# Kernel optimization log

Measured on AMD Instinct MI355X. Metric: run time of the kernel, lower is better.

Reference implementation:

```python
import jax, jax.numpy as jnp
import numpy as np


def setup_inputs() -> dict:
    key = jax.random.key(0)
    k1, k2 = jax.random.split(key)
    ns, nd, n_classes = 16384, 2048, 1000
    x = jax.random.normal(k1, (ns, nd), dtype=jnp.float32)
    # prototype means for all seen classes (seen_c == n_classes)
    means = jax.random.normal(k2, (n_classes, nd), dtype=jnp.float32)
    return {"x": x, "means": means, "n_classes": n_classes}


def reference(x, means, n_classes):
    # Original: per-sample dist = -means @ x[s]; argmin(dist) == argmax(means @ x[s]).
    # Batched: one GEMM [ns, nd] x [nd, seen_c] -> scores [ns, seen_c].
    ns = x.shape[0]
    xf = x.reshape(ns, -1)
    scores = jnp.einsum('nd,cd->nc', xf, means)  # [ns, seen_c]
    classpred = jnp.argmax(scores, axis=1)       # argmin of -scores
    out = jax.nn.one_hot(classpred, n_classes, dtype=jnp.float32)  # [ns, n_classes]
    return out
```

## Files before the change

### kernel.cpp

```cpp
#include <hip/hip_runtime.h>
#include <math.h>

#define NS 16384
#define ND 2048
#define NC 1000
#define NCPAD 1024

typedef _Float16 f16x8 __attribute__((ext_vector_type(8)));
typedef _Float16 f16x4 __attribute__((ext_vector_type(4)));
typedef __fp16   h16x2 __attribute__((ext_vector_type(2)));
typedef float f32x4  __attribute__((ext_vector_type(4)));

#define DELTA 2.5f

#define WS_FAST 37748736ull

__device__ __forceinline__ void gl_lds16_h(const _Float16* g, _Float16* l) {
    __builtin_amdgcn_global_load_lds(
        (const __attribute__((address_space(1))) unsigned int*)g,
        (__attribute__((address_space(3))) unsigned int*)l, 16, 0, 0);
}

__device__ __forceinline__ f16x8 cvt8(const f32x4 a0, const f32x4 a1) {
    const h16x2 h01 = __builtin_amdgcn_cvt_pkrtz(a0[0], a0[1]);
    const h16x2 h23 = __builtin_amdgcn_cvt_pkrtz(a0[2], a0[3]);
    const h16x2 h45 = __builtin_amdgcn_cvt_pkrtz(a1[0], a1[1]);
    const h16x2 h67 = __builtin_amdgcn_cvt_pkrtz(a1[2], a1[3]);
    f16x8 h;
    h[0]=(_Float16)h01[0]; h[1]=(_Float16)h01[1]; h[2]=(_Float16)h23[0]; h[3]=(_Float16)h23[1];
    h[4]=(_Float16)h45[0]; h[5]=(_Float16)h45[1]; h[6]=(_Float16)h67[0]; h[7]=(_Float16)h67[1];
    return h;
}

__global__ __launch_bounds__(256)
void cvt_m_kernel(const float* __restrict__ src, _Float16* __restrict__ hi)
{
    const int i = blockIdx.x * 256 + threadIdx.x;
    const int row = (i * 4) >> 11;
    float4 v = make_float4(0.f, 0.f, 0.f, 0.f);
    if (row < NC) v = ((const float4*)src)[i];
    f16x4 h;
    h[0] = (_Float16)v.x; h[1] = (_Float16)v.y;
    h[2] = (_Float16)v.z; h[3] = (_Float16)v.w;
    ((f16x4*)hi)[i] = h;
}

__device__ __forceinline__ void stage_unitB(const _Float16* __restrict__ src,
                                            size_t g0, _Float16* dstbase,
                                            int srcT, int kkh, int tid)
{
#pragma unroll
    for (int q = 0; q < 2; ++q) {
        const int slot = q * 512 + tid;
        const int row  = slot >> 2;
        const int g    = (slot & 3) ^ ((row >> 1) & 3);
        gl_lds16_h(src + ((g0 + (size_t)row) << 11) + srcT * 64 + kkh * 32 + g * 8,
                   dstbase + (size_t)(q * 512 + ((tid >> 6) << 6)) * 8);
    }
}

__global__ __launch_bounds__(512, 2)
void gemm256_kernel(const float* __restrict__ x,
                    const _Float16* __restrict__ mhi,
                    _Float16* __restrict__ sc)
{
    __shared__ _Float16 sA[2][2][256 * 32];
    __shared__ _Float16 sB[2][2][256 * 32];

    const int tid  = threadIdx.x;
    const int lane = tid & 63;
    const int w    = tid >> 6;
    const int wm   = w >> 2;
    const int wn   = w & 3;
    const int quad = lane >> 4, l16 = lane & 15;

    const int orig = blockIdx.x + (blockIdx.y << 2);
    const int nid  = ((orig & 7) << 5) + (orig >> 3);
    const size_t gm0 = (size_t)(nid >> 2) * 256;
    const size_t gn0 = (size_t)(nid & 3) * 256;

    const int arow = tid >> 1;
    const int aseg = tid & 1;
    const int as   = (arow >> 1) & 3;
    const int ap0  = (aseg * 2)     ^ as;
    const int ap1  = (aseg * 2 + 1) ^ as;
    const float* xA = x + ((gm0 + (size_t)arow) << 11) + aseg * 16;

    f32x4 acc[8][4] = {};

    stage_unitB(mhi, gn0, &sB[0][0][0], 0, 0, tid);
    stage_unitB(mhi, gn0, &sB[0][1][0], 0, 1, tid);
    {
        f32x4 v0[4], v1[4];
#pragma unroll
        for (int q = 0; q < 4; ++q) v0[q] = *(const f32x4*)(xA + q * 4);
#pragma unroll
        for (int q = 0; q < 4; ++q) v1[q] = *(const f32x4*)(xA + 32 + q * 4);
        const f16x8 h00 = cvt8(v0[0], v0[1]), h01 = cvt8(v0[2], v0[3]);
        const f16x8 h10 = cvt8(v1[0], v1[1]), h11 = cvt8(v1[2], v1[3]);
        *(f16x8*)&sA[0][0][arow * 32 + ap0 * 8] = h00;
        *(f16x8*)&sA[0][0][arow * 32 + ap1 * 8] = h01;
        *(f16x8*)&sA[0][1][arow * 32 + ap0 * 8] = h10;
        *(f16x8*)&sA[0][1][arow * 32 + ap1 * 8] = h11;
    }
    asm volatile("s_waitcnt vmcnt(0) lgkmcnt(0)" ::: "memory");
    __builtin_amdgcn_s_barrier();

    for (int kt = 0; kt < 32; ++kt) {
        const int par = kt & 1, nxt = par ^ 1;
        const int srcT = (kt + 1 < 32) ? kt + 1 : 31;
        const float* xT = xA + srcT * 64;

        f16x8 a0[4], a1[4], b0[4];
#pragma unroll
        for (int i = 0; i < 4; ++i) {
            const int r0 = wm * 128 + i * 16 + l16;
            const int r1 = r0 + 64;
            a0[i] = *(const f16x8*)&sA[par][0][r0 * 32 + (quad ^ ((r0 >> 1) & 3)) * 8];
            a1[i] = *(const f16x8*)&sA[par][0][r1 * 32 + (quad ^ ((r1 >> 1) & 3)) * 8];
        }
#pragma unroll
        for (int j = 0; j < 4; ++j) {
            const int br = wn * 64 + j * 16 + l16;
            b0[j] = *(const f16x8*)&sB[par][0][br * 32 + (quad ^ ((br >> 1) & 3)) * 8];
        }
        stage_unitB(mhi, gn0, &sB[nxt][0][0], srcT, 0, tid);
        stage_unitB(mhi, gn0, &sB[nxt][1][0], srcT, 1, tid);
        f32x4 av0[4];
#pragma unroll
        for (int q = 0; q < 4; ++q) av0[q] = *(const f32x4*)(xT + q * 4);
        __builtin_amdgcn_sched_barrier(0);
        __builtin_amdgcn_s_setprio(1);
#pragma unroll
        for (int i = 0; i < 4; ++i)
#pragma unroll
            for (int j = 0; j < 4; ++j)
                acc[i][j] = __builtin_amdgcn_mfma_f32_16x16x32_f16(a0[i], b0[j], acc[i][j], 0, 0, 0);
#pragma unroll
        for (int i = 0; i < 4; ++i)
#pragma unroll
            for (int j = 0; j < 4; ++j)
                acc[4 + i][j] = __builtin_amdgcn_mfma_f32_16x16x32_f16(a1[i], b0[j], acc[4 + i][j], 0, 0, 0);
        __builtin_amdgcn_s_setprio(0);

        f16x8 c0[4], c1[4], b1[4];
#pragma unroll
        for (int i = 0; i < 4; ++i) {
            const int r0 = wm * 128 + i * 16 + l16;
            const int r1 = r0 + 64;
            c0[i] = *(const f16x8*)&sA[par][1][r0 * 32 + (quad ^ ((r0 >> 1) & 3)) * 8];
            c1[i] = *(const f16x8*)&sA[par][1][r1 * 32 + (quad ^ ((r1 >> 1) & 3)) * 8];
        }
#pragma unroll
        for (int j = 0; j < 4; ++j) {
            const int br = wn * 64 + j * 16 + l16;
            b1[j] = *(const f16x8*)&sB[par][1][br * 32 + (quad ^ ((br >> 1) & 3)) * 8];
        }
        {
            const f16x8 h0 = cvt8(av0[0], av0[1]), h1 = cvt8(av0[2], av0[3]);
            *(f16x8*)&sA[nxt][0][arow * 32 + ap0 * 8] = h0;
            *(f16x8*)&sA[nxt][0][arow * 32 + ap1 * 8] = h1;
        }
        f32x4 av1[4];
#pragma unroll
        for (int q = 0; q < 4; ++q) av1[q] = *(const f32x4*)(xT + 32 + q * 4);
        __builtin_amdgcn_sched_barrier(0);
        __builtin_amdgcn_s_setprio(1);
#pragma unroll
        for (int i = 0; i < 4; ++i)
#pragma unroll
            for (int j = 0; j < 4; ++j)
                acc[i][j] = __builtin_amdgcn_mfma_f32_16x16x32_f16(c0[i], b1[j], acc[i][j], 0, 0, 0);
#pragma unroll
        for (int i = 0; i < 4; ++i)
#pragma unroll
            for (int j = 0; j < 4; ++j)
                acc[4 + i][j] = __builtin_amdgcn_mfma_f32_16x16x32_f16(c1[i], b1[j], acc[4 + i][j], 0, 0, 0);
        __builtin_amdgcn_s_setprio(0);
        {
            const f16x8 h0 = cvt8(av1[0], av1[1]), h1 = cvt8(av1[2], av1[3]);
            *(f16x8*)&sA[nxt][1][arow * 32 + ap0 * 8] = h0;
            *(f16x8*)&sA[nxt][1][arow * 32 + ap1 * 8] = h1;
        }
        asm volatile("s_waitcnt vmcnt(0) lgkmcnt(0)" ::: "memory");
        __builtin_amdgcn_s_barrier();
    }

#pragma unroll
    for (int m = 0; m < 8; ++m) {
        const size_t row0 = gm0 + wm * 128 + m * 16 + quad * 4;
#pragma unroll
        for (int j = 0; j < 4; ++j) {
            const size_t col = gn0 + wn * 64 + j * 16 + l16;
#pragma unroll
            for (int r = 0; r < 4; ++r)
                sc[(row0 + r) * NCPAD + col] = (_Float16)acc[m][j][r];
        }
    }
}

__global__ __launch_bounds__(256, 4)
void refine_kernel(const _Float16* __restrict__ sc,
                   const float* __restrict__ x,
                   const float* __restrict__ means,
                   float* __restrict__ out)
{
    const int lane = threadIdx.x & 63;
    const int row  = blockIdx.x * 4 + (threadIdx.x >> 6);

    const f16x8* srow = (const f16x8*)(sc + (size_t)row * NCPAD + lane * 16);
    const f16x8 s0 = srow[0], s1 = srow[1];
    float v[16];
#pragma unroll
    for (int e = 0; e < 8; ++e) { v[e] = (float)s0[e]; v[8 + e] = (float)s1[e]; }

    float mx = -INFINITY;
#pragma unroll
    for (int e = 0; e < 16; ++e) {
        const int c = lane * 16 + e;
        if (c < NC && v[e] > mx) mx = v[e];
    }
#pragma unroll
    for (int off = 1; off < 64; off <<= 1) {
        const float o = __shfl_xor(mx, off);
        if (o > mx) mx = o;
    }
    const float T = mx - DELTA;

    unsigned cm = 0;
#pragma unroll
    for (int e = 0; e < 16; ++e) {
        const int c = lane * 16 + e;
        if (c < NC && v[e] >= T) cm |= (1u << e);
    }

    const unsigned long long bl = __ballot(cm != 0u);
    const int first  = (int)__builtin_ctzll(bl);
    const unsigned cmf = (unsigned)__shfl((int)cm, first);

    int bc;
    if (__builtin_popcountll(bl) == 1 && __builtin_popcount(cmf) == 1) {
        bc = first * 16 + __builtin_ctz(cmf);
    } else {
        const float* xrow = x + ((size_t)row << 11);
        f32x4 xr[8];
#pragma unroll
        for (int it = 0; it < 8; ++it)
            xr[it] = *(const f32x4*)(xrow + it * 256 + lane * 4);

        float bv = -INFINITY;
        bc = 0x7fffffff;
        unsigned long long pend = bl;
        while (pend) {
            const int src = (int)__builtin_ctzll(pend);
            pend &= pend - 1;
            unsigned cms = (unsigned)__shfl((int)cm, src);
            while (cms) {
                const int c = src * 16 + __builtin_ctz(cms);
                cms &= cms - 1;

                const float* mrow = means + ((size_t)c << 11);
                float part = 0.f;
#pragma unroll
                for (int it = 0; it < 8; ++it) {
                    const f32x4 mv = *(const f32x4*)(mrow + it * 256 + lane * 4);
                    part = fmaf(xr[it][0], mv[0], part);
                    part = fmaf(xr[it][1], mv[1], part);
                    part = fmaf(xr[it][2], mv[2], part);
                    part = fmaf(xr[it][3], mv[3], part);
                }
                float s = part;
#pragma unroll
                for (int off = 1; off < 64; off <<= 1) s += __shfl_xor(s, off);

                if (s > bv || (s == bv && c < bc)) { bv = s; bc = c; }
            }
        }
    }

    float4* orow = (float4*)(out + (size_t)row * NC);
#pragma unroll
    for (int i = 0; i < 4; ++i) {
        const int idx = lane + i * 64;
        if (idx < NC / 4) {
            const int cb = idx * 4;
            float4 ov;
            ov.x = (cb     == bc) ? 1.f : 0.f;
            ov.y = (cb + 1 == bc) ? 1.f : 0.f;
            ov.z = (cb + 2 == bc) ? 1.f : 0.f;
            ov.w = (cb + 3 == bc) ? 1.f : 0.f;
            orow[idx] = ov;
        }
    }
}

#define MS 64
#define CS 256
#define KT 32
#define NCHUNK 4

__global__ __launch_bounds__(256, 1)
void nnc_fp32_kernel(const float* __restrict__ x,
                     const float* __restrict__ means,
                     float* __restrict__ out)
{
    __shared__ float xs[MS * KT];
    __shared__ float msh[CS * KT];
    __shared__ float rbest[MS * 33];
    __shared__ int   ridx[MS * 33];
    __shared__ int   widx[MS];

    const int tid = threadIdx.x;
    const int tx  = tid & 31;
    const int ty  = tid >> 5;
    const int s0  = blockIdx.x * MS;
    const int m0  = ty * 8;
    const int cL  = tx * 8;

    float best[8];
    int   bidx[8];
#pragma unroll
    for (int i = 0; i < 8; ++i) { best[i] = -INFINITY; bidx[i] = 0; }

    const int kslot = tid & 7;
    const int rrow  = tid >> 3;

    for (int chunk = 0; chunk < NCHUNK; ++chunk) {
        const int c0 = chunk * CS;
        float acc[8][8];
#pragma unroll
        for (int i = 0; i < 8; ++i)
#pragma unroll
            for (int j = 0; j < 8; ++j) acc[i][j] = 0.0f;

        for (int k0 = 0; k0 < ND; k0 += KT) {
#pragma unroll
            for (int r = 0; r < 2; ++r) {
                const int m = rrow + r * 32;
                const float4 v = *(const float4*)(x + (size_t)(s0 + m) * ND + k0 + kslot * 4);
                *(float4*)(xs + m * KT + kslot * 4) = v;
            }
#pragma unroll
            for (int r = 0; r < 8; ++r) {
                const int c  = rrow + r * 32;
                const int cg = c0 + c;
                float4 v = make_float4(0.f, 0.f, 0.f, 0.f);
                if (cg < NC) v = *(const float4*)(means + (size_t)cg * ND + k0 + kslot * 4);
                const int pslot = (kslot + (c >> 3)) & 7;
                *(float4*)(msh + c * KT + pslot * 4) = v;
            }
            __syncthreads();
#pragma unroll
            for (int k4 = 0; k4 < KT / 4; ++k4) {
                float4 a[8], b[8];
                const int boff = ((k4 + tx) & 7) * 4;
#pragma unroll
                for (int i = 0; i < 8; ++i) a[i] = *(const float4*)(xs + (m0 + i) * KT + k4 * 4);
#pragma unroll
                for (int j = 0; j < 8; ++j) b[j] = *(const float4*)(msh + (cL + j) * KT + boff);
#pragma unroll
                for (int i = 0; i < 8; ++i)
#pragma unroll
                    for (int j = 0; j < 8; ++j) {
                        acc[i][j] = fmaf(a[i].x, b[j].x, acc[i][j]);
                        acc[i][j] = fmaf(a[i].y, b[j].y, acc[i][j]);
                        acc[i][j] = fmaf(a[i].z, b[j].z, acc[i][j]);
                        acc[i][j] = fmaf(a[i].w, b[j].w, acc[i][j]);
                    }
            }
            __syncthreads();
        }
#pragma unroll
        for (int i = 0; i < 8; ++i)
#pragma unroll
            for (int j = 0; j < 8; ++j) {
                const int c = c0 + cL + j;
                const float v = acc[i][j];
                if (c < NC && (v > best[i] || (v == best[i] && c < bidx[i]))) {
                    best[i] = v; bidx[i] = c;
                }
            }
    }
#pragma unroll
    for (int i = 0; i < 8; ++i) {
        rbest[(m0 + i) * 33 + tx] = best[i];
        ridx[(m0 + i) * 33 + tx]  = bidx[i];
    }
    __syncthreads();
    if (tid < MS) {
        float bv = rbest[tid * 33];
        int   bc = ridx[tid * 33];
        for (int t = 1; t < 32; ++t) {
            const float v = rbest[tid * 33 + t];
            const int   c = ridx[tid * 33 + t];
            if (v > bv || (v == bv && c < bc)) { bv = v; bc = c; }
        }
        widx[tid] = bc;
    }
    __syncthreads();
    if (tid < 250) {
        const int cbase = tid * 4;
        for (int m = 0; m < MS; ++m) {
            const int w = widx[m];
            float4 v;
            v.x = (cbase == w) ? 1.f : 0.f;
            v.y = (cbase + 1 == w) ? 1.f : 0.f;
            v.z = (cbase + 2 == w) ? 1.f : 0.f;
            v.w = (cbase + 3 == w) ? 1.f : 0.f;
            *(float4*)(out + (size_t)(s0 + m) * NC + cbase) = v;
        }
    }
}

extern "C" void kernel_launch(void* const* d_in, const int* in_sizes, int n_in,
                              void* d_out, int out_size, void* d_ws, size_t ws_size,
                              hipStream_t stream) {
    const float* x     = (const float*)d_in[0];
    const float* means = (const float*)d_in[1];
    float* out         = (float*)d_out;

    if (ws_size >= WS_FAST) {
        char* ws = (char*)d_ws;
        _Float16* mhi = (_Float16*)ws;
        _Float16* sc  = (_Float16*)(ws + (4ull << 20));

        cvt_m_kernel<<<dim3(NCPAD * ND / 4 / 256), dim3(256), 0, stream>>>(means, mhi);
        gemm256_kernel<<<dim3(NCPAD / 256, NS / 256), dim3(512), 0, stream>>>(x, mhi, sc);
        refine_kernel<<<dim3(NS / 4), dim3(256), 0, stream>>>(sc, x, means, out);
    } else {
        nnc_fp32_kernel<<<dim3(NS / MS), dim3(256), 0, stream>>>(x, means, out);
    }
}
```

Baseline: 306.3 us.

## Prefetch fp32 A tile two stages ahead with partial vmcnt waits

The fp32 x loads for the A operand are now issued two k-steps ahead into a register buffer instead of one. Each iteration converts and stores the previous prefetch to LDS, then issues the next loads. The barrier wait drops to vmcnt(8), so those 8 loads can stay in flight across the barrier while the B direct-to-LDS loads are still waited on. The aim is to hide global load latency for the A operand behind more MFMA work. In exchange it needs 8 more live vector registers and relies on the vmcnt count being exact.

```diff
diff --git a/kernel.cpp b/kernel.cpp
--- a/kernel.cpp
+++ b/kernel.cpp
@@ -87,29 +87,37 @@
     const float* xA = x + ((gm0 + (size_t)arow) << 11) + aseg * 16;
 
     f32x4 acc[8][4] = {};
-
+    f32x4 av[8];
+
+#pragma unroll
+    for (int q = 0; q < 4; ++q) av[q]     = *(const f32x4*)(xA + q * 4);
+#pragma unroll
+    for (int q = 0; q < 4; ++q) av[4 + q] = *(const f32x4*)(xA + 32 + q * 4);
     stage_unitB(mhi, gn0, &sB[0][0][0], 0, 0, tid);
     stage_unitB(mhi, gn0, &sB[0][1][0], 0, 1, tid);
     {
-        f32x4 v0[4], v1[4];
-#pragma unroll
-        for (int q = 0; q < 4; ++q) v0[q] = *(const f32x4*)(xA + q * 4);
-#pragma unroll
-        for (int q = 0; q < 4; ++q) v1[q] = *(const f32x4*)(xA + 32 + q * 4);
-        const f16x8 h00 = cvt8(v0[0], v0[1]), h01 = cvt8(v0[2], v0[3]);
-        const f16x8 h10 = cvt8(v1[0], v1[1]), h11 = cvt8(v1[2], v1[3]);
+        const f16x8 h00 = cvt8(av[0], av[1]), h01 = cvt8(av[2], av[3]);
+        const f16x8 h10 = cvt8(av[4], av[5]), h11 = cvt8(av[6], av[7]);
         *(f16x8*)&sA[0][0][arow * 32 + ap0 * 8] = h00;
         *(f16x8*)&sA[0][0][arow * 32 + ap1 * 8] = h01;
         *(f16x8*)&sA[0][1][arow * 32 + ap0 * 8] = h10;
         *(f16x8*)&sA[0][1][arow * 32 + ap1 * 8] = h11;
     }
-    asm volatile("s_waitcnt vmcnt(0) lgkmcnt(0)" ::: "memory");
+    __builtin_amdgcn_sched_barrier(0);
+    {
+        const float* xT1 = xA + 64;
+#pragma unroll
+        for (int q = 0; q < 4; ++q) av[q]     = *(const f32x4*)(xT1 + q * 4);
+#pragma unroll
+        for (int q = 0; q < 4; ++q) av[4 + q] = *(const f32x4*)(xT1 + 32 + q * 4);
+    }
+    asm volatile("s_waitcnt vmcnt(8) lgkmcnt(0)" ::: "memory");
     __builtin_amdgcn_s_barrier();
 
     for (int kt = 0; kt < 32; ++kt) {
         const int par = kt & 1, nxt = par ^ 1;
-        const int srcT = (kt + 1 < 32) ? kt + 1 : 31;
-        const float* xT = xA + srcT * 64;
+        const int srcB = (kt + 1 < 32) ? kt + 1 : 31;
+        const int srcA = (kt + 2 < 32) ? kt + 2 : 31;
 
         f16x8 a0[4], a1[4], b0[4];
 #pragma unroll
@@ -124,11 +132,8 @@
             const int br = wn * 64 + j * 16 + l16;
             b0[j] = *(const f16x8*)&sB[par][0][br * 32 + (quad ^ ((br >> 1) & 3)) * 8];
         }
-        stage_unitB(mhi, gn0, &sB[nxt][0][0], srcT, 0, tid);
-        stage_unitB(mhi, gn0, &sB[nxt][1][0], srcT, 1, tid);
-        f32x4 av0[4];
-#pragma unroll
-        for (int q = 0; q < 4; ++q) av0[q] = *(const f32x4*)(xT + q * 4);
+        stage_unitB(mhi, gn0, &sB[nxt][0][0], srcB, 0, tid);
+        stage_unitB(mhi, gn0, &sB[nxt][1][0], srcB, 1, tid);
         __builtin_amdgcn_sched_barrier(0);
         __builtin_amdgcn_s_setprio(1);
 #pragma unroll
@@ -157,13 +162,21 @@
             b1[j] = *(const f16x8*)&sB[par][1][br * 32 + (quad ^ ((br >> 1) & 3)) * 8];
         }
         {
-            const f16x8 h0 = cvt8(av0[0], av0[1]), h1 = cvt8(av0[2], av0[3]);
-            *(f16x8*)&sA[nxt][0][arow * 32 + ap0 * 8] = h0;
-            *(f16x8*)&sA[nxt][0][arow * 32 + ap1 * 8] = h1;
-        }
-        f32x4 av1[4];
-#pragma unroll
-        for (int q = 0; q < 4; ++q) av1[q] = *(const f32x4*)(xT + 32 + q * 4);
+            const f16x8 h00 = cvt8(av[0], av[1]), h01 = cvt8(av[2], av[3]);
+            const f16x8 h10 = cvt8(av[4], av[5]), h11 = cvt8(av[6], av[7]);
+            *(f16x8*)&sA[nxt][0][arow * 32 + ap0 * 8] = h00;
+            *(f16x8*)&sA[nxt][0][arow * 32 + ap1 * 8] = h01;
+            *(f16x8*)&sA[nxt][1][arow * 32 + ap0 * 8] = h10;
+            *(f16x8*)&sA[nxt][1][arow * 32 + ap1 * 8] = h11;
+        }
+        __builtin_amdgcn_sched_barrier(0);
+        {
+            const float* xT = xA + srcA * 64;
+#pragma unroll
+            for (int q = 0; q < 4; ++q) av[q]     = *(const f32x4*)(xT + q * 4);
+#pragma unroll
+            for (int q = 0; q < 4; ++q) av[4 + q] = *(const f32x4*)(xT + 32 + q * 4);
+        }
         __builtin_amdgcn_sched_barrier(0);
         __builtin_amdgcn_s_setprio(1);
 #pragma unroll
@@ -177,12 +190,7 @@
             for (int j = 0; j < 4; ++j)
                 acc[4 + i][j] = __builtin_amdgcn_mfma_f32_16x16x32_f16(c1[i], b1[j], acc[4 + i][j], 0, 0, 0);
         __builtin_amdgcn_s_setprio(0);
-        {
-            const f16x8 h0 = cvt8(av1[0], av1[1]), h1 = cvt8(av1[2], av1[3]);
-            *(f16x8*)&sA[nxt][1][arow * 32 + ap0 * 8] = h0;
-            *(f16x8*)&sA[nxt][1][arow * 32 + ap1 * 8] = h1;
-        }
-        asm volatile("s_waitcnt vmcnt(0) lgkmcnt(0)" ::: "memory");
+        asm volatile("s_waitcnt vmcnt(8) lgkmcnt(0)" ::: "memory");
         __builtin_amdgcn_s_barrier();
     }
 
```

Result: faster. 279.7 us (-8.7%).
